# Kernel tuning notes

Hardware: AMD Instinct MI355X
Metric: run time of the kernel (lower is better)

The kernel has to match this reference:

```python
import jax, jax.numpy as jnp
import numpy as np
import math

B, S, D, H, L = 4, 2048, 512, 8, 2
HD = D // H
NG = (3, 4, 5)
V = 30000          # n_gram_vocab_size
BASE = 31          # rolling hash base
NPATCH = 16
PLEN = S // NPATCH


def _ln(x, w, b, eps):
    m = x.mean(-1, keepdims=True)
    v = ((x - m) ** 2).mean(-1, keepdims=True)
    return (x - m) * jax.lax.rsqrt(v + eps) * w + b


def setup_inputs() -> dict:
    key = jax.random.key(0)
    ks = jax.random.split(key, 16)

    def nrm(i, shape, std=0.02):
        return jax.random.normal(ks[i], shape, dtype=jnp.float32) * std

    return {
        "byte_seq": jax.random.randint(ks[0], (B, S), 0, 256, dtype=jnp.int32),
        "patch_boundaries": jnp.arange(NPATCH + 1, dtype=jnp.int32) * PLEN,
        "byte_emb": nrm(1, (256, D), 1.0 / math.sqrt(D)),
        "ng_emb": nrm(2, (len(NG), V, D)),
        "tl_qkv_w": nrm(3, (L, 3 * D, D)),
        "tl_qkv_b": jnp.zeros((L, 3 * D), jnp.float32),
        "tl_out_w": nrm(4, (L, D, D)),
        "tl_out_b": jnp.zeros((L, D), jnp.float32),
        "tl_ln1_w": jnp.ones((L, D), jnp.float32),
        "tl_ln1_b": jnp.zeros((L, D), jnp.float32),
        "tl_ln2_w": jnp.ones((L, D), jnp.float32),
        "tl_ln2_b": jnp.zeros((L, D), jnp.float32),
        "tl_ff1_w": nrm(5, (L, 4 * D, D)),
        "tl_ff1_b": jnp.zeros((L, 4 * D), jnp.float32),
        "tl_ff2_w": nrm(6, (L, D, 4 * D)),
        "tl_ff2_b": jnp.zeros((L, D), jnp.float32),
        "ca_qkv_w": nrm(7, (3 * D, D)),
        "ca_qkv_b": jnp.zeros((3 * D,), jnp.float32),
        "ca_out_w": nrm(8, (D, D)),
        "ca_out_b": jnp.zeros((D,), jnp.float32),
        "ca_ln_w": jnp.ones((D,), jnp.float32),
        "ca_ln_b": jnp.zeros((D,), jnp.float32),
        "norm_w": jnp.ones((D,), jnp.float32),
        "norm_b": jnp.zeros((D,), jnp.float32),
    }


def _forward(byte_seq, patch_boundaries, byte_emb, ng_emb,
             tl_qkv_w, tl_qkv_b, tl_out_w, tl_out_b,
             tl_ln1_w, tl_ln1_b, tl_ln2_w, tl_ln2_b,
             tl_ff1_w, tl_ff1_b, tl_ff2_w, tl_ff2_b,
             ca_qkv_w, ca_qkv_b, ca_out_w, ca_out_b, ca_ln_w, ca_ln_b,
             norm_w, norm_b):
    x = byte_emb[byte_seq]                                  # [B,S,D]

    # n-gram rolling hash == polynomial hash mod V; computed in parallel
    # as windowed dot products with modular base powers (exact same values
    # as the sequential rolling-update loop in the torch code).
    ng_scale = 1.0 / (len(NG) + 1)
    for idx, n in enumerate(NG):
        powers = jnp.array([pow(BASE, n - 1 - i, V) for i in range(n)],
                           dtype=byte_seq.dtype)
        windows = jnp.stack([byte_seq[:, j:S - n + 1 + j] for j in range(n)],
                            axis=-1)                        # [B,S-n+1,n]
        h = (windows * powers).sum(-1) % V                   # [B,S-n+1]
        x = x.at[:, n - 1:].add(ng_emb[idx][h] * ng_scale)

    scale = 1.0 / math.sqrt(HD)
    neg = jnp.where(jnp.triu(jnp.ones((S, S), dtype=bool), 1),
                    -jnp.inf, 0.0).astype(x.dtype)           # causal additive mask

    # post-norm TransformerEncoderLayer (relu activation, dropout=0/eval)
    for l in range(L):
        qkv = x @ tl_qkv_w[l].T + tl_qkv_b[l]                # [B,S,3D]
        q, k, v = jnp.split(qkv, 3, axis=-1)
        q = q.reshape(B, S, H, HD).transpose(0, 2, 1, 3)
        k = k.reshape(B, S, H, HD).transpose(0, 2, 1, 3)
        v = v.reshape(B, S, H, HD).transpose(0, 2, 1, 3)
        scores = jnp.einsum('bhqd,bhkd->bhqk', q, k) * scale + neg
        a = jax.nn.softmax(scores, axis=-1)
        o = jnp.einsum('bhqk,bhkd->bhqd', a, v).transpose(0, 2, 1, 3).reshape(B, S, D)
        o = o @ tl_out_w[l].T + tl_out_b[l]
        x = _ln(x + o, tl_ln1_w[l], tl_ln1_b[l], 1e-5)
        ff = jax.nn.relu(x @ tl_ff1_w[l].T + tl_ff1_b[l]) @ tl_ff2_w[l].T + tl_ff2_b[l]
        x = _ln(x + ff, tl_ln2_w[l], tl_ln2_b[l], 1e-5)

    # uniform patch boundaries -> vectorized patch cross-attention
    npatch = patch_boundaries.shape[0] - 1
    plen = S // npatch
    xp = x.reshape(B, npatch, plen, D)
    query = xp.mean(axis=2)                                  # [B,P,D]
    qn = _ln(query, ca_ln_w, ca_ln_b, 1e-6)
    kvn = _ln(xp, ca_ln_w, ca_ln_b, 1e-6)
    wq, wk, wv = jnp.split(ca_qkv_w, 3, axis=0)
    bq, bk, bv = jnp.split(ca_qkv_b, 3)
    q = (qn @ wq.T + bq).reshape(B, npatch, H, HD)
    k = (kvn @ wk.T + bk).reshape(B, npatch, plen, H, HD)
    v = (kvn @ wv.T + bv).reshape(B, npatch, plen, H, HD)
    s = jnp.einsum('bphd,bplhd->bphl', q, k) * scale
    a = jax.nn.softmax(s, axis=-1)
    o = jnp.einsum('bphl,bplhd->bphd', a, v).reshape(B, npatch, D)
    patches = query + (o @ ca_out_w.T + ca_out_b)

    return _ln(x, norm_w, norm_b, 1e-6), _ln(patches, norm_w, norm_b, 1e-6)


def reference(byte_seq, patch_boundaries, byte_emb, ng_emb,
              tl_qkv_w, tl_qkv_b, tl_out_w, tl_out_b,
              tl_ln1_w, tl_ln1_b, tl_ln2_w, tl_ln2_b,
              tl_ff1_w, tl_ff1_b, tl_ff2_w, tl_ff2_b,
              ca_qkv_w, ca_qkv_b, ca_out_w, ca_out_b, ca_ln_w, ca_ln_b,
              norm_w, norm_b):
    return _forward(byte_seq, patch_boundaries, byte_emb, ng_emb,
                    tl_qkv_w, tl_qkv_b, tl_out_w, tl_out_b,
                    tl_ln1_w, tl_ln1_b, tl_ln2_w, tl_ln2_b,
                    tl_ff1_w, tl_ff1_b, tl_ff2_w, tl_ff2_b,
                    ca_qkv_w, ca_qkv_b, ca_out_w, ca_out_b, ca_ln_w, ca_ln_b,
                    norm_w, norm_b)
```

## Files before the change

### kernel.cpp

```cpp
#include <hip/hip_runtime.h>
#include <hip/hip_bf16.h>

#define B_ 4
#define S_ 2048
#define D_ 512
#define H_ 8
#define HD_ 64
#define L_ 2
#define V_ 30000
#define NPATCH_ 16
#define PLEN_ 128

typedef short bf16x8 __attribute__((ext_vector_type(8)));
typedef float f32x4 __attribute__((ext_vector_type(4)));

__device__ __forceinline__ unsigned short f2bf(float f) {
    unsigned u = __float_as_uint(f);
    return (unsigned short)((u + 0x7FFFu + ((u >> 16) & 1u)) >> 16);
}

#define C0_ (2*1536*512/4)
#define C1_ (2*512*512/4)
#define C2_ (2*2048*512/4)
#define C3_ (2*512*2048/4)
#define C4_ (1024*512/4)
__global__ __launch_bounds__(256) void cast5_kernel(
    const float* __restrict__ s0, const float* __restrict__ s1,
    const float* __restrict__ s2, const float* __restrict__ s3,
    const float* __restrict__ s4,
    unsigned short* __restrict__ d0, unsigned short* __restrict__ d1,
    unsigned short* __restrict__ d2, unsigned short* __restrict__ d3,
    unsigned short* __restrict__ d4)
{
    int i = blockIdx.x * 256 + threadIdx.x;
    const float* s; unsigned short* d;
    if      (i < C0_)                  { s = s0; d = d0; }
    else if ((i -= C0_) < C1_)         { s = s1; d = d1; }
    else if ((i -= C1_) < C2_)         { s = s2; d = d2; }
    else if ((i -= C2_) < C3_)         { s = s3; d = d3; }
    else if ((i -= C3_) < C4_)         { s = s4; d = d4; }
    else return;
    const float4 v = *reinterpret_cast<const float4*>(s + (size_t)i * 4);
    ushort4 o;
    o.x = f2bf(v.x); o.y = f2bf(v.y); o.z = f2bf(v.z); o.w = f2bf(v.w);
    *reinterpret_cast<ushort4*>(d + (size_t)i * 4) = o;
}

__global__ __launch_bounds__(128) void embed_ngram_kernel(
    const int* __restrict__ bytes, const float* __restrict__ byte_emb,
    const float* __restrict__ ng_emb, float* __restrict__ x,
    unsigned short* __restrict__ xb)
{
    const int bs = blockIdx.x;
    const int s  = bs % S_;
    const int b  = bs / S_;
    const int d  = threadIdx.x * 4;
    const int* brow = bytes + (size_t)b * S_;

    const int c = brow[s];
    float4 v = *reinterpret_cast<const float4*>(byte_emb + (size_t)c * D_ + d);

    if (s >= 2) {
        int h = (brow[s-2]*961 + brow[s-1]*31 + brow[s]) % V_;
        const float4 g = *reinterpret_cast<const float4*>(ng_emb + ((size_t)0*V_ + h)*D_ + d);
        v.x += 0.25f*g.x; v.y += 0.25f*g.y; v.z += 0.25f*g.z; v.w += 0.25f*g.w;
    }
    if (s >= 3) {
        int h = (brow[s-3]*29791 + brow[s-2]*961 + brow[s-1]*31 + brow[s]) % V_;
        const float4 g = *reinterpret_cast<const float4*>(ng_emb + ((size_t)1*V_ + h)*D_ + d);
        v.x += 0.25f*g.x; v.y += 0.25f*g.y; v.z += 0.25f*g.z; v.w += 0.25f*g.w;
    }
    if (s >= 4) {
        int h = (brow[s-4]*23521 + brow[s-3]*29791 + brow[s-2]*961 + brow[s-1]*31 + brow[s]) % V_;
        const float4 g = *reinterpret_cast<const float4*>(ng_emb + ((size_t)2*V_ + h)*D_ + d);
        v.x += 0.25f*g.x; v.y += 0.25f*g.y; v.z += 0.25f*g.z; v.w += 0.25f*g.w;
    }
    *reinterpret_cast<float4*>(x + (size_t)bs * D_ + d) = v;
    ushort4 o;
    o.x = f2bf(v.x); o.y = f2bf(v.y); o.z = f2bf(v.z); o.w = f2bf(v.w);
    *reinterpret_cast<ushort4*>(xb + (size_t)bs * D_ + d) = o;
}

template<int DO_RELU, int BF16OUT, int BN>
__global__ __launch_bounds__(256) void mgemm_kernel(
    const unsigned short* __restrict__ Xb, const unsigned short* __restrict__ Wb,
    const float* __restrict__ bias, void* __restrict__ Yout,
    int M, int N, int K)
{
    constexpr int NT  = BN / 32;
    constexpr int NLB = BN / 32;
    __shared__ unsigned short As[128*64];
    __shared__ unsigned short Bs[BN*64];

    const int t    = threadIdx.x;
    const int lane = t & 63;
    const int w    = t >> 6;
    const int bm   = blockIdx.y * 128, bn = blockIdx.x * BN;
    const int l15  = lane & 15, lg = lane >> 4;
    const int wr   = w >> 1, wc = w & 1;

    int srow[4], scol[4];
#pragma unroll
    for (int i = 0; i < 4; ++i) {
        const int off = w*1024 + i*4096 + lane*16;
        srow[i] = off >> 7;
        scol[i] = ((off >> 4) & 7) ^ (srow[i] & 7);
    }

    f32x4 acc[4][NT];
#pragma unroll
    for (int mt = 0; mt < 4; ++mt)
#pragma unroll
        for (int nt = 0; nt < NT; ++nt) acc[mt][nt] = (f32x4){0.f,0.f,0.f,0.f};

    for (int kt = 0; kt < K; kt += 64) {
#pragma unroll
        for (int i = 0; i < 4; ++i) {
            const unsigned short* gA = Xb + (size_t)(bm + srow[i]) * K + kt + scol[i]*8;
            __builtin_amdgcn_global_load_lds(
                (const __attribute__((address_space(1))) void*)gA,
                (__attribute__((address_space(3))) void*)&As[w*512 + i*2048], 16, 0, 0);
        }
#pragma unroll
        for (int i = 0; i < NLB; ++i) {
            const unsigned short* gB = Wb + (size_t)(bn + srow[i]) * K + kt + scol[i]*8;
            __builtin_amdgcn_global_load_lds(
                (const __attribute__((address_space(1))) void*)gB,
                (__attribute__((address_space(3))) void*)&Bs[w*512 + i*2048], 16, 0, 0);
        }
        __syncthreads();

#pragma unroll
        for (int ks = 0; ks < 2; ++ks) {
            const int c16 = (ks*4 + lg) ^ (l15 & 7);
            bf16x8 a[4], b[NT];
#pragma unroll
            for (int mt = 0; mt < 4; ++mt)
                a[mt] = *reinterpret_cast<const bf16x8*>(&As[(wr*64 + mt*16 + l15)*64 + c16*8]);
#pragma unroll
            for (int nt = 0; nt < NT; ++nt)
                b[nt] = *reinterpret_cast<const bf16x8*>(&Bs[(wc*(BN/2) + nt*16 + l15)*64 + c16*8]);
#pragma unroll
            for (int mt = 0; mt < 4; ++mt)
#pragma unroll
                for (int nt = 0; nt < NT; ++nt)
                    acc[mt][nt] = __builtin_amdgcn_mfma_f32_16x16x32_bf16(
                        a[mt], b[nt], acc[mt][nt], 0, 0, 0);
        }
        __syncthreads();
    }

    float bv[NT];
#pragma unroll
    for (int nt = 0; nt < NT; ++nt) bv[nt] = bias[bn + wc*(BN/2) + nt*16 + l15];

#pragma unroll
    for (int mt = 0; mt < 4; ++mt) {
#pragma unroll
        for (int nt = 0; nt < NT; ++nt) {
            const int n = bn + wc*(BN/2) + nt*16 + l15;
#pragma unroll
            for (int r = 0; r < 4; ++r) {
                const int m = bm + wr*64 + mt*16 + 4*lg + r;
                float v = acc[mt][nt][r] + bv[nt];
                if (DO_RELU) v = fmaxf(v, 0.f);
                if (BF16OUT)
                    ((unsigned short*)Yout)[(size_t)m * N + n] = f2bf(v);
                else
                    ((float*)Yout)[(size_t)m * N + n] = v;
            }
        }
    }
}

__global__ __launch_bounds__(256) void gemm_kernel(
    const float* __restrict__ X, const float* __restrict__ W,
    const float* __restrict__ bias, const float* __restrict__ resid,
    float* __restrict__ Y, int M, int N, int K, int do_relu)
{
    __shared__ float As[16][68];
    __shared__ float Bs[16][68];
    const int tid = threadIdx.x;
    const int bm = blockIdx.y * 64, bn = blockIdx.x * 64;
    const int ty = tid >> 4, tx = tid & 15;
    const int lrow = tid >> 2, lc4 = (tid & 3) * 4;

    float acc[4][4];
#pragma unroll
    for (int i = 0; i < 4; ++i)
#pragma unroll
        for (int j = 0; j < 4; ++j) acc[i][j] = 0.f;

    for (int k0 = 0; k0 < K; k0 += 16) {
        const float4 xv = *reinterpret_cast<const float4*>(X + (size_t)(bm + lrow) * K + k0 + lc4);
        const float4 wv = *reinterpret_cast<const float4*>(W + (size_t)(bn + lrow) * K + k0 + lc4);
        __syncthreads();
        As[lc4+0][lrow] = xv.x; As[lc4+1][lrow] = xv.y;
        As[lc4+2][lrow] = xv.z; As[lc4+3][lrow] = xv.w;
        Bs[lc4+0][lrow] = wv.x; Bs[lc4+1][lrow] = wv.y;
        Bs[lc4+2][lrow] = wv.z; Bs[lc4+3][lrow] = wv.w;
        __syncthreads();
#pragma unroll
        for (int kk = 0; kk < 16; ++kk) {
            float a0 = As[kk][ty*4+0], a1 = As[kk][ty*4+1], a2 = As[kk][ty*4+2], a3 = As[kk][ty*4+3];
            float b0 = Bs[kk][tx*4+0], b1 = Bs[kk][tx*4+1], b2 = Bs[kk][tx*4+2], b3 = Bs[kk][tx*4+3];
            acc[0][0] += a0*b0; acc[0][1] += a0*b1; acc[0][2] += a0*b2; acc[0][3] += a0*b3;
            acc[1][0] += a1*b0; acc[1][1] += a1*b1; acc[1][2] += a1*b2; acc[1][3] += a1*b3;
            acc[2][0] += a2*b0; acc[2][1] += a2*b1; acc[2][2] += a2*b2; acc[2][3] += a2*b3;
            acc[3][0] += a3*b0; acc[3][1] += a3*b1; acc[3][2] += a3*b2; acc[3][3] += a3*b3;
        }
    }

#pragma unroll
    for (int i = 0; i < 4; ++i) {
        const int m = bm + ty*4 + i;
#pragma unroll
        for (int j = 0; j < 4; ++j) {
            const int n = bn + tx*4 + j;
            float v = acc[i][j] + bias[n];
            if (do_relu) v = fmaxf(v, 0.f);
            if (resid) v += resid[(size_t)m * N + n];
            Y[(size_t)m * N + n] = v;
        }
    }
}

__global__ __launch_bounds__(256) void attn_mfma_kernel(
    const unsigned short* __restrict__ qkvb, unsigned short* __restrict__ ob)
{
    __shared__ unsigned short Ks[64*72];
    __shared__ unsigned short Vt[64*72];
    __shared__ unsigned short Plds[4*16*72];

    const int t    = threadIdx.x;
    const int lane = t & 63;
    const int w    = t >> 6;
    const int qp   = blockIdx.x;
    const int bh   = blockIdx.y;
    const int h    = bh & 7;
    const int b    = bh >> 3;

    const unsigned short* base = qkvb + (size_t)b * S_ * 1536;
    const int l15 = lane & 15, lg = lane >> 4;
    const int skey = t >> 2, sd0 = (t & 3) * 16;
    const int sg = sd0 >> 4;
    const int scs = ((skey >> 3) ^ sg) * 8 + (skey & 7);
    unsigned short* pw_base = Plds + w*16*72;

    bf16x8 k0r, k1r, v0r, v1r;
#define LOADREG(KT) { \
        const unsigned short* srcK_ = base + (size_t)((KT) + skey) * 1536 + 512 + h*64 + sd0; \
        k0r = *reinterpret_cast<const bf16x8*>(srcK_); \
        k1r = *reinterpret_cast<const bf16x8*>(srcK_ + 8); \
        v0r = *reinterpret_cast<const bf16x8*>(srcK_ + 512); \
        v1r = *reinterpret_cast<const bf16x8*>(srcK_ + 520); }

    LOADREG(0);

#pragma unroll
    for (int half = 0; half < 2; ++half) {
        const int qb  = half ? (31 - qp) : qp;
        const int q0w = qb * 64 + w * 16;

        bf16x8 qf0, qf1;
        {
            const unsigned short* qr = base + (size_t)(q0w + l15) * 1536 + h*64 + lg*8;
            qf0 = *reinterpret_cast<const bf16x8*>(qr);
            qf1 = *reinterpret_cast<const bf16x8*>(qr + 32);
        }

        f32x4 oacc[4];
#pragma unroll
        for (int i = 0; i < 4; ++i) oacc[i] = (f32x4){0.f,0.f,0.f,0.f};
        float mrow[4] = {-INFINITY,-INFINITY,-INFINITY,-INFINITY};
        float lrow[4] = {0.f,0.f,0.f,0.f};

        const int ntiles = qb + 1;
        for (int tile = 0; tile < ntiles; ++tile) {
            const int kt = tile * 64;
            __syncthreads();
            *reinterpret_cast<bf16x8*>(&Ks[skey*72 + sd0])     = k0r;
            *reinterpret_cast<bf16x8*>(&Ks[skey*72 + sd0 + 8]) = k1r;
#pragma unroll
            for (int j = 0; j < 8; ++j) Vt[(sd0+j)*72 + scs]   = (unsigned short)v0r[j];
#pragma unroll
            for (int j = 0; j < 8; ++j) Vt[(sd0+8+j)*72 + scs] = (unsigned short)v1r[j];
            __syncthreads();
            const int nkt = (tile + 1 < ntiles) ? (kt + 64) : 0;
            LOADREG(nkt);

            f32x4 sacc[4];
#pragma unroll
            for (int kt16 = 0; kt16 < 4; ++kt16) {
                sacc[kt16] = (f32x4){0.f,0.f,0.f,0.f};
                const unsigned short* kp = &Ks[(kt16*16 + l15)*72 + lg*8];
                bf16x8 k0 = *reinterpret_cast<const bf16x8*>(kp);
                bf16x8 k1 = *reinterpret_cast<const bf16x8*>(kp + 32);
                sacc[kt16] = __builtin_amdgcn_mfma_f32_16x16x32_bf16(qf0, k0, sacc[kt16], 0, 0, 0);
                sacc[kt16] = __builtin_amdgcn_mfma_f32_16x16x32_bf16(qf1, k1, sacc[kt16], 0, 0, 0);
            }

            const bool diag = (tile == ntiles - 1);
            float sv[4][4];
#pragma unroll
            for (int kt16 = 0; kt16 < 4; ++kt16) {
#pragma unroll
                for (int r = 0; r < 4; ++r) {
                    float s = sacc[kt16][r] * 0.125f;
                    if (diag) {
                        const int key = kt + kt16*16 + l15;
                        const int q   = q0w + 4*lg + r;
                        if (key > q) s = -INFINITY;
                    }
                    sv[kt16][r] = s;
                }
            }
#pragma unroll
            for (int r = 0; r < 4; ++r) {
                float tm = fmaxf(fmaxf(sv[0][r], sv[1][r]), fmaxf(sv[2][r], sv[3][r]));
#pragma unroll
                for (int off = 8; off; off >>= 1) tm = fmaxf(tm, __shfl_xor(tm, off, 64));
                const float nm = fmaxf(mrow[r], tm);
                const float al = __expf(mrow[r] - nm);
                mrow[r] = nm;
                float ps = 0.f;
#pragma unroll
                for (int kt16 = 0; kt16 < 4; ++kt16) {
                    const float p = __expf(sv[kt16][r] - nm);
                    ps += p;
                    pw_base[(4*lg + r)*72 + kt16*16 + l15] = f2bf(p);
                }
#pragma unroll
                for (int off = 8; off; off >>= 1) ps += __shfl_xor(ps, off, 64);
                lrow[r] = lrow[r]*al + ps;
#pragma unroll
                for (int dt = 0; dt < 4; ++dt) oacc[dt][r] *= al;
            }

            const unsigned short* pr = &pw_base[l15*72 + lg*8];
            bf16x8 pa0 = *reinterpret_cast<const bf16x8*>(pr);
            bf16x8 pa1 = *reinterpret_cast<const bf16x8*>(pr + 32);
#pragma unroll
            for (int dt = 0; dt < 4; ++dt) {
                const unsigned short* vp = &Vt[(dt*16 + l15)*72 + (lg ^ dt)*8];
                bf16x8 v0 = *reinterpret_cast<const bf16x8*>(vp);
                bf16x8 v1 = *reinterpret_cast<const bf16x8*>(vp + 32);
                oacc[dt] = __builtin_amdgcn_mfma_f32_16x16x32_bf16(pa0, v0, oacc[dt], 0, 0, 0);
                oacc[dt] = __builtin_amdgcn_mfma_f32_16x16x32_bf16(pa1, v1, oacc[dt], 0, 0, 0);
            }
        }

#pragma unroll
        for (int dt = 0; dt < 4; ++dt) {
#pragma unroll
            for (int r = 0; r < 4; ++r) {
                const int q = q0w + 4*lg + r;
                ob[((size_t)b*S_ + q)*D_ + h*64 + dt*16 + l15] = f2bf(oacc[dt][r] / lrow[r]);
            }
        }
    }
#undef LOADREG
}

__global__ __launch_bounds__(256) void ln_kernel(
    float* __restrict__ dst, unsigned short* __restrict__ dst2,
    const float* __restrict__ src, const float* __restrict__ add,
    const float* __restrict__ w, const float* __restrict__ b, float eps)
{
    const int row = blockIdx.x, tid = threadIdx.x;
    const int lane = tid & 63, wave = tid >> 6;
    float2 v = *reinterpret_cast<const float2*>(src + (size_t)row * D_ + tid*2);
    if (add) {
        float2 a = *reinterpret_cast<const float2*>(add + (size_t)row * D_ + tid*2);
        v.x += a.x; v.y += a.y;
    }
    __shared__ float red[8];
    float s = v.x + v.y;
#pragma unroll
    for (int off = 32; off; off >>= 1) s += __shfl_xor(s, off, 64);
    if (lane == 0) red[wave] = s;
    __syncthreads();
    const float mean = (red[0]+red[1]+red[2]+red[3]) * (1.f/D_);
    const float d0 = v.x - mean, d1 = v.y - mean;
    float sq = d0*d0 + d1*d1;
#pragma unroll
    for (int off = 32; off; off >>= 1) sq += __shfl_xor(sq, off, 64);
    if (lane == 0) red[4+wave] = sq;
    __syncthreads();
    const float var = (red[4]+red[5]+red[6]+red[7]) * (1.f/D_);
    const float inv = rsqrtf(var + eps);
    const float o0 = d0*inv*w[tid*2] + b[tid*2];
    const float o1 = d1*inv*w[tid*2+1] + b[tid*2+1];
    *reinterpret_cast<float2*>(dst + (size_t)row * D_ + tid*2) = make_float2(o0, o1);
    if (dst2) {
        ushort2 u; u.x = f2bf(o0); u.y = f2bf(o1);
        *reinterpret_cast<ushort2*>(dst2 + (size_t)row * D_ + tid*2) = u;
    }
}

__global__ __launch_bounds__(256) void meanpool_kernel(
    const float* __restrict__ x, float* __restrict__ query)
{
    const int bp = blockIdx.x;
    const int d = threadIdx.x * 2;
    const float* base = x + (size_t)bp * PLEN_ * D_ + d;
    float s0 = 0.f, s1 = 0.f;
    for (int l = 0; l < PLEN_; ++l) {
        float2 v = *reinterpret_cast<const float2*>(base + (size_t)l * D_);
        s0 += v.x; s1 += v.y;
    }
    query[(size_t)bp*D_ + d]     = s0 * (1.f/PLEN_);
    query[(size_t)bp*D_ + d + 1] = s1 * (1.f/PLEN_);
}

__global__ __launch_bounds__(256) void patch_attn_kernel(
    const float* __restrict__ qbuf, const float* __restrict__ kv,
    float* __restrict__ o)
{
    const int wid  = blockIdx.x * 4 + (threadIdx.x >> 6);
    const int lane = threadIdx.x & 63;
    const int h  = wid % H_;
    const int bp = wid / H_;
    const float qv = qbuf[(size_t)bp*D_ + h*HD_ + lane] * 0.125f;
    const float* base = kv + (size_t)bp * PLEN_ * 1024 + h*HD_;

    float m = -INFINITY, l = 0.f, acc = 0.f;
    for (int t = 0; t < PLEN_; ++t) {
        const float* row = base + (size_t)t * 1024;
        float s = qv * row[lane];
#pragma unroll
        for (int off = 32; off; off >>= 1) s += __shfl_xor(s, off, 64);
        const float vv = row[512 + lane];
        const float nm = fmaxf(m, s);
        const float al = __expf(m - nm);
        const float p  = __expf(s - nm);
        l = l * al + p;
        acc = acc * al + p * vv;
        m = nm;
    }
    o[(size_t)bp*D_ + h*HD_ + lane] = acc / l;
}

extern "C" void kernel_launch(void* const* d_in, const int* in_sizes, int n_in,
                              void* d_out, int out_size, void* d_ws, size_t ws_size,
                              hipStream_t stream)
{
    const int*   byte_seq = (const int*)d_in[0];
    const float* byte_emb = (const float*)d_in[2];
    const float* ng_emb   = (const float*)d_in[3];
    const float* qkv_w = (const float*)d_in[4];
    const float* qkv_b = (const float*)d_in[5];
    const float* out_w = (const float*)d_in[6];
    const float* out_b = (const float*)d_in[7];
    const float* ln1_w = (const float*)d_in[8];
    const float* ln1_b = (const float*)d_in[9];
    const float* ln2_w = (const float*)d_in[10];
    const float* ln2_b = (const float*)d_in[11];
    const float* ff1_w = (const float*)d_in[12];
    const float* ff1_b = (const float*)d_in[13];
    const float* ff2_w = (const float*)d_in[14];
    const float* ff2_b = (const float*)d_in[15];
    const float* ca_qkv_w = (const float*)d_in[16];
    const float* ca_qkv_b = (const float*)d_in[17];
    const float* ca_out_w = (const float*)d_in[18];
    const float* ca_out_b = (const float*)d_in[19];
    const float* ca_ln_w  = (const float*)d_in[20];
    const float* ca_ln_b  = (const float*)d_in[21];
    const float* norm_w   = (const float*)d_in[22];
    const float* norm_b   = (const float*)d_in[23];
    float* out = (float*)d_out;

    char* ws = (char*)d_ws;
    const size_t MB = 1024*1024;
    float*          x     = (float*)(ws);
    char*           bufA  = ws + 16*MB;
    float*          bufB  = (float*)(ws + 48*MB);
    unsigned short* ob    = (unsigned short*)(ws + 64*MB);
    unsigned short* xb    = (unsigned short*)(ws + 72*MB);
    unsigned short* qkvw_b = (unsigned short*)(ws + 80*MB);
    unsigned short* outw_b = (unsigned short*)(ws + 83*MB);
    unsigned short* ff1w_b = (unsigned short*)(ws + 84*MB);
    unsigned short* ff2w_b = (unsigned short*)(ws + 88*MB);
    unsigned short* kvw_b  = (unsigned short*)(ws + 92*MB);
    float* query   = (float*)(ws + 93*MB);
    float* qn      = query + 64*512;
    float* qsm     = qn + 64*512;
    float* oca     = qsm + 64*512;
    float* patches = oca + 64*512;

    unsigned short* qkvb = (unsigned short*)bufA;
    unsigned short* ff1b = (unsigned short*)bufA;
    float*          kvf  = (float*)bufA;

    const int M = B_ * S_;

    cast5_kernel<<<(C0_+C1_+C2_+C3_+C4_+255)/256, 256, 0, stream>>>(
        qkv_w, out_w, ff1_w, ff2_w, ca_qkv_w + 512*512,
        qkvw_b, outw_b, ff1w_b, ff2w_b, kvw_b);

    embed_ngram_kernel<<<M, 128, 0, stream>>>(byte_seq, byte_emb, ng_emb, x, xb);

    for (int l = 0; l < L_; ++l) {
        mgemm_kernel<0,1,128><<<dim3(1536/128, M/128), 256, 0, stream>>>(
            xb, qkvw_b + (size_t)l*1536*D_, qkv_b + l*1536, qkvb, M, 1536, D_);
        attn_mfma_kernel<<<dim3(S_/128, B_*H_), 256, 0, stream>>>(qkvb, ob);
        mgemm_kernel<0,0,64><<<dim3(D_/64, M/128), 256, 0, stream>>>(
            ob, outw_b + (size_t)l*D_*D_, out_b + l*D_, bufB, M, D_, D_);
        ln_kernel<<<M, 256, 0, stream>>>(x, xb, x, bufB, ln1_w + l*D_, ln1_b + l*D_, 1e-5f);
        mgemm_kernel<1,1,128><<<dim3(2048/128, M/128), 256, 0, stream>>>(
            xb, ff1w_b + (size_t)l*2048*D_, ff1_b + l*2048, ff1b, M, 2048, D_);
        mgemm_kernel<0,0,64><<<dim3(D_/64, M/128), 256, 0, stream>>>(
            ff1b, ff2w_b + (size_t)l*D_*2048, ff2_b + l*D_, bufB, M, D_, 2048);
        ln_kernel<<<M, 256, 0, stream>>>(x, xb, x, bufB, ln2_w + l*D_, ln2_b + l*D_, 1e-5f);
    }

    meanpool_kernel<<<B_*NPATCH_, 256, 0, stream>>>(x, query);
    ln_kernel<<<B_*NPATCH_, 256, 0, stream>>>(qn, nullptr, query, nullptr, ca_ln_w, ca_ln_b, 1e-6f);
    ln_kernel<<<M, 256, 0, stream>>>(bufB, xb, x, nullptr, ca_ln_w, ca_ln_b, 1e-6f);
    mgemm_kernel<0,0,128><<<dim3(1024/128, M/128), 256, 0, stream>>>(
        xb, kvw_b, ca_qkv_b + 512, kvf, M, 1024, D_);
    gemm_kernel<<<dim3(D_/64, 1), 256, 0, stream>>>(
        qn, ca_qkv_w, ca_qkv_b, nullptr, qsm, 64, D_, D_, 0);
    patch_attn_kernel<<<B_*NPATCH_*H_/4, 256, 0, stream>>>(qsm, kvf, oca);
    gemm_kernel<<<dim3(D_/64, 1), 256, 0, stream>>>(
        oca, ca_out_w, ca_out_b, query, patches, 64, D_, D_, 0);

    ln_kernel<<<M, 256, 0, stream>>>(out, nullptr, x, nullptr, norm_w, norm_b, 1e-6f);
    ln_kernel<<<B_*NPATCH_, 256, 0, stream>>>(
        out + (size_t)M*D_, nullptr, patches, nullptr, norm_w, norm_b, 1e-6f);
}
```

Baseline: 570.6 us.

## Widen attention key tile to 128 and raise wave priority around MFMA

The causal flash-attention kernel now processes 128 keys per iteration instead of 64. K, V-transpose and P buffers in LDS grow to match, each thread stages twice as much K/V data in registers, and the V-transpose swizzle changes. The aim is to halve the number of block-wide barriers and per-tile softmax reductions and to give the MFMA units longer runs. s_setprio hints are added around the MFMA sections. In exchange, odd diagonal tiles now compute masked extra work, register pressure and LDS use go up, and the new swizzle may introduce bank conflicts.

```diff
diff --git a/kernel.cpp b/kernel.cpp
--- a/kernel.cpp
+++ b/kernel.cpp
@@ -228,9 +228,9 @@
 __global__ __launch_bounds__(256) void attn_mfma_kernel(
     const unsigned short* __restrict__ qkvb, unsigned short* __restrict__ ob)
 {
-    __shared__ unsigned short Ks[64*72];
-    __shared__ unsigned short Vt[64*72];
-    __shared__ unsigned short Plds[4*16*72];
+    __shared__ unsigned short Ks[128*72];
+    __shared__ unsigned short Vt[64*136];
+    __shared__ unsigned short Plds[4*16*136];
 
     const int t    = threadIdx.x;
     const int lane = t & 63;
@@ -242,18 +242,22 @@
 
     const unsigned short* base = qkvb + (size_t)b * S_ * 1536;
     const int l15 = lane & 15, lg = lane >> 4;
-    const int skey = t >> 2, sd0 = (t & 3) * 16;
-    const int sg = sd0 >> 4;
-    const int scs = ((skey >> 3) ^ sg) * 8 + (skey & 7);
-    unsigned short* pw_base = Plds + w*16*72;
-
-    bf16x8 k0r, k1r, v0r, v1r;
+    const int skey = t >> 1;
+    const int sd0  = (t & 1) * 32;
+    const int scs  = (((skey >> 3) ^ ((t & 1) << 1)) << 3) + (skey & 7);
+    unsigned short* pw_base = Plds + w*16*136;
+
+    bf16x8 kr0, kr1, kr2, kr3, vr0, vr1, vr2, vr3;
 #define LOADREG(KT) { \
-        const unsigned short* srcK_ = base + (size_t)((KT) + skey) * 1536 + 512 + h*64 + sd0; \
-        k0r = *reinterpret_cast<const bf16x8*>(srcK_); \
-        k1r = *reinterpret_cast<const bf16x8*>(srcK_ + 8); \
-        v0r = *reinterpret_cast<const bf16x8*>(srcK_ + 512); \
-        v1r = *reinterpret_cast<const bf16x8*>(srcK_ + 520); }
+        const unsigned short* p_ = base + (size_t)((KT) + skey) * 1536 + 512 + h*64 + sd0; \
+        kr0 = *reinterpret_cast<const bf16x8*>(p_);       \
+        kr1 = *reinterpret_cast<const bf16x8*>(p_ + 8);   \
+        kr2 = *reinterpret_cast<const bf16x8*>(p_ + 16);  \
+        kr3 = *reinterpret_cast<const bf16x8*>(p_ + 24);  \
+        vr0 = *reinterpret_cast<const bf16x8*>(p_ + 512); \
+        vr1 = *reinterpret_cast<const bf16x8*>(p_ + 520); \
+        vr2 = *reinterpret_cast<const bf16x8*>(p_ + 528); \
+        vr3 = *reinterpret_cast<const bf16x8*>(p_ + 536); }
 
     LOADREG(0);
 
@@ -275,23 +279,30 @@
         float mrow[4] = {-INFINITY,-INFINITY,-INFINITY,-INFINITY};
         float lrow[4] = {0.f,0.f,0.f,0.f};
 
-        const int ntiles = qb + 1;
+        const int ntiles = (qb + 2) >> 1;
         for (int tile = 0; tile < ntiles; ++tile) {
-            const int kt = tile * 64;
+            const int kt = tile * 128;
             __syncthreads();
-            *reinterpret_cast<bf16x8*>(&Ks[skey*72 + sd0])     = k0r;
-            *reinterpret_cast<bf16x8*>(&Ks[skey*72 + sd0 + 8]) = k1r;
-#pragma unroll
-            for (int j = 0; j < 8; ++j) Vt[(sd0+j)*72 + scs]   = (unsigned short)v0r[j];
-#pragma unroll
-            for (int j = 0; j < 8; ++j) Vt[(sd0+8+j)*72 + scs] = (unsigned short)v1r[j];
+            *reinterpret_cast<bf16x8*>(&Ks[skey*72 + sd0])      = kr0;
+            *reinterpret_cast<bf16x8*>(&Ks[skey*72 + sd0 + 8])  = kr1;
+            *reinterpret_cast<bf16x8*>(&Ks[skey*72 + sd0 + 16]) = kr2;
+            *reinterpret_cast<bf16x8*>(&Ks[skey*72 + sd0 + 24]) = kr3;
+#pragma unroll
+            for (int j = 0; j < 8; ++j) Vt[(sd0+j)*136    + scs] = (unsigned short)vr0[j];
+#pragma unroll
+            for (int j = 0; j < 8; ++j) Vt[(sd0+8+j)*136  + scs] = (unsigned short)vr1[j];
+#pragma unroll
+            for (int j = 0; j < 8; ++j) Vt[(sd0+16+j)*136 + scs] = (unsigned short)vr2[j];
+#pragma unroll
+            for (int j = 0; j < 8; ++j) Vt[(sd0+24+j)*136 + scs] = (unsigned short)vr3[j];
             __syncthreads();
-            const int nkt = (tile + 1 < ntiles) ? (kt + 64) : 0;
+            const int nkt = (tile + 1 < ntiles) ? (kt + 128) : 0;
             LOADREG(nkt);
 
-            f32x4 sacc[4];
-#pragma unroll
-            for (int kt16 = 0; kt16 < 4; ++kt16) {
+            f32x4 sacc[8];
+            __builtin_amdgcn_s_setprio(1);
+#pragma unroll
+            for (int kt16 = 0; kt16 < 8; ++kt16) {
                 sacc[kt16] = (f32x4){0.f,0.f,0.f,0.f};
                 const unsigned short* kp = &Ks[(kt16*16 + l15)*72 + lg*8];
                 bf16x8 k0 = *reinterpret_cast<const bf16x8*>(kp);
@@ -299,11 +310,11 @@
                 sacc[kt16] = __builtin_amdgcn_mfma_f32_16x16x32_bf16(qf0, k0, sacc[kt16], 0, 0, 0);
                 sacc[kt16] = __builtin_amdgcn_mfma_f32_16x16x32_bf16(qf1, k1, sacc[kt16], 0, 0, 0);
             }
+            __builtin_amdgcn_s_setprio(0);
 
             const bool diag = (tile == ntiles - 1);
-            float sv[4][4];
-#pragma unroll
-            for (int kt16 = 0; kt16 < 4; ++kt16) {
+#pragma unroll
+            for (int kt16 = 0; kt16 < 8; ++kt16) {
 #pragma unroll
                 for (int r = 0; r < 4; ++r) {
                     float s = sacc[kt16][r] * 0.125f;
@@ -312,12 +323,14 @@
                         const int q   = q0w + 4*lg + r;
                         if (key > q) s = -INFINITY;
                     }
-                    sv[kt16][r] = s;
+                    sacc[kt16][r] = s;
                 }
             }
 #pragma unroll
             for (int r = 0; r < 4; ++r) {
-                float tm = fmaxf(fmaxf(sv[0][r], sv[1][r]), fmaxf(sv[2][r], sv[3][r]));
+                float tm = fmaxf(
+                    fmaxf(fmaxf(sacc[0][r], sacc[1][r]), fmaxf(sacc[2][r], sacc[3][r])),
+                    fmaxf(fmaxf(sacc[4][r], sacc[5][r]), fmaxf(sacc[6][r], sacc[7][r])));
 #pragma unroll
                 for (int off = 8; off; off >>= 1) tm = fmaxf(tm, __shfl_xor(tm, off, 64));
                 const float nm = fmaxf(mrow[r], tm);
@@ -325,10 +338,10 @@
                 mrow[r] = nm;
                 float ps = 0.f;
 #pragma unroll
-                for (int kt16 = 0; kt16 < 4; ++kt16) {
-                    const float p = __expf(sv[kt16][r] - nm);
+                for (int kt16 = 0; kt16 < 8; ++kt16) {
+                    const float p = __expf(sacc[kt16][r] - nm);
                     ps += p;
-                    pw_base[(4*lg + r)*72 + kt16*16 + l15] = f2bf(p);
+                    pw_base[(4*lg + r)*136 + kt16*16 + l15] = f2bf(p);
                 }
 #pragma unroll
                 for (int off = 8; off; off >>= 1) ps += __shfl_xor(ps, off, 64);
@@ -337,17 +350,25 @@
                 for (int dt = 0; dt < 4; ++dt) oacc[dt][r] *= al;
             }
 
-            const unsigned short* pr = &pw_base[l15*72 + lg*8];
+            const unsigned short* pr = &pw_base[l15*136 + lg*8];
             bf16x8 pa0 = *reinterpret_cast<const bf16x8*>(pr);
             bf16x8 pa1 = *reinterpret_cast<const bf16x8*>(pr + 32);
+            bf16x8 pa2 = *reinterpret_cast<const bf16x8*>(pr + 64);
+            bf16x8 pa3 = *reinterpret_cast<const bf16x8*>(pr + 96);
+            __builtin_amdgcn_s_setprio(1);
 #pragma unroll
             for (int dt = 0; dt < 4; ++dt) {
-                const unsigned short* vp = &Vt[(dt*16 + l15)*72 + (lg ^ dt)*8];
-                bf16x8 v0 = *reinterpret_cast<const bf16x8*>(vp);
-                bf16x8 v1 = *reinterpret_cast<const bf16x8*>(vp + 32);
+                const unsigned short* vrow = &Vt[(dt*16 + l15)*136];
+                bf16x8 v0 = *reinterpret_cast<const bf16x8*>(&vrow[(( 0 + lg) ^ (dt & 2))*8]);
+                bf16x8 v1 = *reinterpret_cast<const bf16x8*>(&vrow[(( 4 + lg) ^ (dt & 2))*8]);
+                bf16x8 v2 = *reinterpret_cast<const bf16x8*>(&vrow[(( 8 + lg) ^ (dt & 2))*8]);
+                bf16x8 v3 = *reinterpret_cast<const bf16x8*>(&vrow[((12 + lg) ^ (dt & 2))*8]);
                 oacc[dt] = __builtin_amdgcn_mfma_f32_16x16x32_bf16(pa0, v0, oacc[dt], 0, 0, 0);
                 oacc[dt] = __builtin_amdgcn_mfma_f32_16x16x32_bf16(pa1, v1, oacc[dt], 0, 0, 0);
+                oacc[dt] = __builtin_amdgcn_mfma_f32_16x16x32_bf16(pa2, v2, oacc[dt], 0, 0, 0);
+                oacc[dt] = __builtin_amdgcn_mfma_f32_16x16x32_bf16(pa3, v3, oacc[dt], 0, 0, 0);
             }
+            __builtin_amdgcn_s_setprio(0);
         }
 
 #pragma unroll
```

Result: no change. 568.0 us (-0.5%).
